# Optimization experiments

Measured on AMD Instinct MI355X. Metric: run time of the kernel, lower is better.

The kernel has to match this reference:

```python
import jax, jax.numpy as jnp
import numpy as np

B, S, D, H = 2, 2048, 1024, 16
DK = D // H

def setup_inputs() -> dict:
    key = jax.random.key(0)
    ks = jax.random.split(key, 8)
    return {
        "query": jax.random.normal(ks[0], (B, S, D), dtype=jnp.float32),
        "key": jax.random.normal(ks[1], (B, S, D), dtype=jnp.float32),
        "value": jax.random.normal(ks[2], (B, S, D), dtype=jnp.float32),
        "mask": jax.random.randint(ks[3], (B, S, S), 0, 2, dtype=jnp.int32),
        "w_q": jax.random.normal(ks[4], (D, D), dtype=jnp.float32) * (D ** -0.5),
        "w_k": jax.random.normal(ks[5], (D, D), dtype=jnp.float32) * (D ** -0.5),
        "w_v": jax.random.normal(ks[6], (D, D), dtype=jnp.float32) * (D ** -0.5),
        "w_o": jax.random.normal(ks[7], (D, D), dtype=jnp.float32) * (D ** -0.5),
    }

def reference(query, key, value, mask, w_q, w_k, w_v, w_o):
    b, s, d = query.shape
    # Linear projections (torch nn.Linear: x @ W.T); here w_* are [out, in]
    Q = jnp.einsum('bsd,ed->bse', query, w_q).reshape(b, s, H, DK).transpose(0, 2, 1, 3)
    K = jnp.einsum('bsd,ed->bse', key, w_k).reshape(b, s, H, DK).transpose(0, 2, 1, 3)
    V = jnp.einsum('bsd,ed->bse', value, w_v).reshape(b, s, H, DK).transpose(0, 2, 1, 3)
    scale = jnp.float32(DK ** 0.5)
    scores = jnp.einsum('bhqd,bhkd->bhqk', Q, K) / scale  # [B,H,S,S]
    scores = jnp.where(mask[:, None, :, :] == 0, jnp.float32(-1e9), scores)
    attn = jax.nn.softmax(scores, axis=-1)  # dropout p=0 -> identity
    out = jnp.einsum('bhqk,bhkd->bhqd', attn, V)  # [B,H,S,DK]
    out = out.transpose(0, 2, 1, 3).reshape(b, s, d)
    return jnp.einsum('bsd,ed->bse', out, w_o)
```

## Files before the change

### kernel.cpp

```cpp
#include <hip/hip_runtime.h>
#include <stdint.h>

#define B_ 2
#define S_ 2048
#define D_ 1024
#define H_ 16
#define DK_ 64

typedef __attribute__((ext_vector_type(8))) short short8;
typedef __attribute__((ext_vector_type(4))) float f32x4;

__device__ __forceinline__ short f2bf(float f) {
    uint32_t u = __float_as_uint(f);
    return (short)((u + 0x7FFFu + ((u >> 16) & 1u)) >> 16);
}

__device__ __forceinline__ float fexp2(float x) {
    float r;
    asm("v_exp_f32 %0, %1" : "=v"(r) : "v"(x));
    return r;
}

__device__ __forceinline__ uint32_t cvt_pk_bf16(float lo, float hi) {
    uint32_t r;
    asm("v_cvt_pk_bf16_f32 %0, %1, %2" : "=v"(r) : "v"(lo), "v"(hi));
    return r;
}

#define GLOAD16(gptr, lptr)                                                      \
    __builtin_amdgcn_global_load_lds(                                            \
        (const __attribute__((address_space(1))) void*)(gptr),                   \
        (__attribute__((address_space(3))) void*)(lptr), 16, 0, 0)

__global__ __launch_bounds__(256) void prep(const float* __restrict__ q,
                                            const float* __restrict__ k,
                                            const float* __restrict__ v,
                                            const float* __restrict__ wq,
                                            const float* __restrict__ wk,
                                            const float* __restrict__ wv,
                                            const float* __restrict__ wo,
                                            const int* __restrict__ mask,
                                            short* __restrict__ qb, short* __restrict__ kb,
                                            short* __restrict__ vb,
                                            short* __restrict__ wqb, short* __restrict__ wkb,
                                            short* __restrict__ wvb, short* __restrict__ wob,
                                            uint32_t* __restrict__ packed,
                                            float* __restrict__ lut) {
    int bid = blockIdx.x;
    int tid = threadIdx.x;
    if (bid < 8192) {
        const float* in;
        short* out;
        int i;
        if (bid < 6144) {
            int sel = bid >> 11;
            i = (bid & 2047) * 256 + tid;
            in = (sel == 0) ? q : (sel == 1) ? k : v;
            out = (sel == 0) ? qb : (sel == 1) ? kb : vb;
        } else {
            int idx = bid - 6144;
            int sel = idx >> 9;
            i = (idx & 511) * 256 + tid;
            in = (sel == 0) ? wq : (sel == 1) ? wk : (sel == 2) ? wv : wo;
            out = (sel == 0) ? wqb : (sel == 1) ? wkb : (sel == 2) ? wvb : wob;
            if (idx == 0 && tid < 64) {
                int e = tid >> 2, r = tid & 3;
                lut[tid] = ((e >> r) & 1) ? 0.0f : -8.0e9f;
            }
        }
        const float4* p = ((const float4*)in) + (size_t)i * 2;
        float4 x = p[0], y = p[1];
        short8 o;
        o[0] = f2bf(x.x); o[1] = f2bf(x.y); o[2] = f2bf(x.z); o[3] = f2bf(x.w);
        o[4] = f2bf(y.x); o[5] = f2bf(y.y); o[6] = f2bf(y.z); o[7] = f2bf(y.w);
        *(((short8*)out) + i) = o;
    } else {
        size_t t = (size_t)(bid - 8192) * 256 + tid;
        int4 m = ((const int4*)mask)[t];
        uint32_t nib = (m.x != 0 ? 1u : 0u) | (m.y != 0 ? 2u : 0u) |
                       (m.z != 0 ? 4u : 0u) | (m.w != 0 ? 8u : 0u);
        int lane = tid & 63;
        uint32_t vv = nib << ((lane & 7) * 4);
        vv |= __shfl_xor(vv, 1);
        vv |= __shfl_xor(vv, 2);
        vv |= __shfl_xor(vv, 4);
        if ((lane & 7) == 0) packed[t >> 3] = vv;
    }
}

#define GEMM_BODY(A, W, C, F32OUT, Mv, Nv, Kv)                                              \
    __shared__ short As[128 * 32];                                                          \
    __shared__ short Bs[128 * 32];                                                          \
    const int tid = threadIdx.x;                                                            \
    const int lane = tid & 63;                                                              \
    const int w = tid >> 6;                                                                 \
    const int wm = w >> 1, wn = w & 1;                                                      \
    const int l_ = blockIdx.x + (blockIdx.y << 3);                                          \
    const int xcd_ = l_ & 7, ii_ = l_ >> 3;                                                 \
    const int mBase = ((xcd_ << 2) + (ii_ >> 3)) * 128;                                     \
    const int nBase = (ii_ & 7) * 128;                                                      \
    f32x4 acc[4][4];                                                                        \
    _Pragma("unroll") for (int i = 0; i < 4; i++)                                           \
        _Pragma("unroll") for (int j = 0; j < 4; j++) acc[i][j] = (f32x4)0.f;               \
    const int srow = lane >> 2;                                                             \
    const int sslot = lane & 3;                                                             \
    for (int k0 = 0; k0 < Kv; k0 += 32) {                                                   \
        _Pragma("unroll") for (int i = 0; i < 2; ++i) {                                     \
            int seg = w * 2 + i;                                                            \
            int row = seg * 16 + srow;                                                      \
            const short* ga = A + (size_t)(mBase + row) * Kv + k0 + sslot * 8;              \
            GLOAD16(ga, (char*)As + seg * 1024);                                            \
            const short* gb = W + (size_t)(nBase + row) * Kv + k0 + sslot * 8;              \
            GLOAD16(gb, (char*)Bs + seg * 1024);                                            \
        }                                                                                   \
        asm volatile("s_waitcnt vmcnt(0)" ::: "memory");                                    \
        __syncthreads();                                                                    \
        short8 af[4], bfv[4];                                                               \
        _Pragma("unroll") for (int mi = 0; mi < 4; mi++)                                    \
            af[mi] = *(const short8*)&As[(wm * 64 + mi * 16 + (lane & 15)) * 32 + (lane >> 4) * 8]; \
        _Pragma("unroll") for (int ni = 0; ni < 4; ni++)                                    \
            bfv[ni] = *(const short8*)&Bs[(wn * 64 + ni * 16 + (lane & 15)) * 32 + (lane >> 4) * 8]; \
        _Pragma("unroll") for (int mi = 0; mi < 4; mi++)                                    \
            _Pragma("unroll") for (int ni = 0; ni < 4; ni++)                                \
                acc[mi][ni] = __builtin_amdgcn_mfma_f32_16x16x32_bf16(af[mi], bfv[ni], acc[mi][ni], 0, 0, 0); \
        __syncthreads();                                                                    \
    }                                                                                       \
    _Pragma("unroll") for (int mi = 0; mi < 4; mi++)                                        \
        _Pragma("unroll") for (int ni = 0; ni < 4; ni++)                                    \
            _Pragma("unroll") for (int r = 0; r < 4; r++) {                                 \
                int row = mBase + wm * 64 + mi * 16 + (lane >> 4) * 4 + r;                  \
                int col = nBase + wn * 64 + ni * 16 + (lane & 15);                          \
                float v = acc[mi][ni][r];                                                   \
                if (F32OUT) ((float*)C)[(size_t)row * Nv + col] = v;                        \
                else        ((short*)C)[(size_t)row * Nv + col] = f2bf(v);                  \
            }

__global__ __launch_bounds__(256) void gemm3_nt(const short* __restrict__ A0, const short* __restrict__ W0, short* __restrict__ C0,
                                                const short* __restrict__ A1, const short* __restrict__ W1, short* __restrict__ C1,
                                                const short* __restrict__ A2, const short* __restrict__ W2, short* __restrict__ C2) {
    const int z = blockIdx.z;
    const short* A = (z == 0) ? A0 : (z == 1) ? A1 : A2;
    const short* W = (z == 0) ? W0 : (z == 1) ? W1 : W2;
    short* C = (z == 0) ? C0 : (z == 1) ? C1 : C2;
    GEMM_BODY(A, W, C, 0, (B_ * S_), D_, D_)
}

__global__ __launch_bounds__(256) void gemm_out(const short* __restrict__ A,
                                                const short* __restrict__ W,
                                                float* __restrict__ C) {
    GEMM_BODY(A, W, C, 1, (B_ * S_), D_, D_)
}

__global__ __launch_bounds__(256) void transpose_v(const short* __restrict__ Vp,
                                                   short* __restrict__ Vt) {
    __shared__ short t[64 * 72];
    int bid = blockIdx.x;
    int bh = bid >> 5;
    int st = bid & 31;
    int b = bh >> 4, h = bh & 15;
    int sBase = st * 64;
    int tid = threadIdx.x;
#pragma unroll
    for (int i = 0; i < 2; i++) {
        int ci = i * 256 + tid;
        int sr = ci >> 3, sl = ci & 7;
        short8 v = *(const short8*)&Vp[(size_t)(b * S_ + sBase + sr) * D_ + h * 64 + sl * 8];
#pragma unroll
        for (int j = 0; j < 8; j++) t[(sl * 8 + j) * 72 + sr] = v[j];
    }
    __syncthreads();
#pragma unroll
    for (int i = 0; i < 2; i++) {
        int ci = i * 256 + tid;
        int dk = ci >> 3, sl = ci & 7;
        short8 o = *(const short8*)&t[dk * 72 + sl * 8];
        *(short8*)&Vt[(size_t)((b * H_ + h) * 64 + dk) * S_ + sBase + sl * 8] = o;
    }
}

__global__ __launch_bounds__(512) void attn_kernel(const short* __restrict__ Qp,
                                                   const short* __restrict__ Kp,
                                                   const short* __restrict__ Vt,
                                                   const uint32_t* __restrict__ mp,
                                                   const float* __restrict__ lutg,
                                                   short* __restrict__ Op) {
    __shared__ short Ks[2][2][64 * 64];
    __shared__ short Vs[2][2][64 * 64];
    const int l_ = blockIdx.x + (blockIdx.y << 4);
    const int bh = ((l_ & 7) << 2) + (l_ >> 7);
    const int qt = (l_ >> 3) & 15;
    const int b = bh >> 4, h = bh & 15;
    const int qBase = qt * 128;
    const int tid = threadIdx.x, lane = tid & 63, w = tid >> 6;
    const int lg = lane >> 4;
    const int li = lane & 15;
    const float c1 = 0.18033688011112042f;

    const int q = qBase + w * 16 + li;

    short8 qf[2];
#pragma unroll
    for (int ks = 0; ks < 2; ks++)
        qf[ks] = *(const short8*)&Qp[(size_t)(b * S_ + q) * D_ + h * 64 + lg * 8 + ks * 32];

    const int r0 = tid >> 3, sl = tid & 7;
    const int gs = sl ^ (r0 & 7);
    const short* kgb = Kp + ((size_t)(b * S_) + r0) * D_ + h * 64 + gs * 8;
    const short* vgb = Vt + ((size_t)bh * 64 + r0) * S_ + gs * 8;
    const uint32_t* mrow = mp + ((size_t)(b * S_) + q) * 64;
    char* ldsK = (char*)&Ks[0][0][0];
    char* ldsV = (char*)&Vs[0][0][0];
    const int woff = w * 1024;

#pragma unroll
    for (int st = 0; st < 2; st++) {
        GLOAD16(kgb + (size_t)(st * 64) * D_, ldsK + st * 8192 + woff);
        GLOAD16(vgb + st * 64, ldsV + st * 8192 + woff);
    }
    uint4 mw4 = *(const uint4*)mrow;
    asm volatile("s_waitcnt vmcnt(0)" ::: "memory");
    __syncthreads();

    float m_r = -1e30f, l_r = 0.f;
    f32x4 acc[4];
#pragma unroll
    for (int g = 0; g < 4; g++) acc[g] = (f32x4)0.f;

    int cur = 0;

    for (int kt = 0; kt < S_ / 128; ++kt) {
        uint32_t mwarr[4] = {mw4.x, mw4.y, mw4.z, mw4.w};
        f32x4 msk[8];
#pragma unroll
        for (int nt = 0; nt < 8; nt++) {
            uint32_t wd = mwarr[nt >> 1];
            uint32_t nib = (wd >> (((nt & 1) << 4) + (lg << 2))) & 0xFu;
            msk[nt] = *(const f32x4*)&lutg[nib * 4];
        }

        uint4 mwn;
        if (kt < S_ / 128 - 1) {
            const int boff = (cur ^ 1) * 16384 + woff;
#pragma unroll
            for (int st = 0; st < 2; st++) {
                const size_t kr = (size_t)((kt + 1) * 128 + st * 64);
                GLOAD16(kgb + kr * D_, ldsK + boff + st * 8192);
                GLOAD16(vgb + kr, ldsV + boff + st * 8192);
            }
            mwn = *(const uint4*)&mrow[(kt + 1) * 4];
        }

        f32x4 sc[8];
        __builtin_amdgcn_s_setprio(1);
#pragma unroll
        for (int st = 0; st < 2; st++)
#pragma unroll
            for (int ntl = 0; ntl < 4; ntl++) {
                f32x4 c = msk[st * 4 + ntl];
#pragma unroll
                for (int ks = 0; ks < 2; ks++) {
                    short8 kf = *(const short8*)&Ks[cur][st][(ntl * 16 + li) * 64 + (((lg + ks * 4) ^ (li & 7)) << 3)];
                    c = __builtin_amdgcn_mfma_f32_16x16x32_bf16(kf, qf[ks], c, 0, 0, 0);
                }
                sc[st * 4 + ntl] = c;
            }
        __builtin_amdgcn_s_setprio(0);

        float t0 = fmaxf(fmaxf(sc[0][0], sc[0][1]), fmaxf(sc[0][2], sc[0][3]));
        float t1 = fmaxf(fmaxf(sc[1][0], sc[1][1]), fmaxf(sc[1][2], sc[1][3]));
        float t2 = fmaxf(fmaxf(sc[2][0], sc[2][1]), fmaxf(sc[2][2], sc[2][3]));
        float t3 = fmaxf(fmaxf(sc[3][0], sc[3][1]), fmaxf(sc[3][2], sc[3][3]));
        float t4 = fmaxf(fmaxf(sc[4][0], sc[4][1]), fmaxf(sc[4][2], sc[4][3]));
        float t5 = fmaxf(fmaxf(sc[5][0], sc[5][1]), fmaxf(sc[5][2], sc[5][3]));
        float t6 = fmaxf(fmaxf(sc[6][0], sc[6][1]), fmaxf(sc[6][2], sc[6][3]));
        float t7 = fmaxf(fmaxf(sc[7][0], sc[7][1]), fmaxf(sc[7][2], sc[7][3]));
        float tm = fmaxf(fmaxf(fmaxf(t0, t1), fmaxf(t2, t3)),
                         fmaxf(fmaxf(t4, t5), fmaxf(t6, t7)));
        tm = fmaxf(tm, __shfl_xor(tm, 16));
        tm = fmaxf(tm, __shfl_xor(tm, 32));

        if (__any((tm - m_r) * c1 > 10.0f)) {
            float mn = fmaxf(m_r, tm);
            float alpha = fexp2((m_r - mn) * c1);
            m_r = mn;
            l_r *= alpha;
#pragma unroll
            for (int g = 0; g < 4; g++) acc[g] *= alpha;
        }
        float mc = m_r * c1;

        uint32_t u[8][2];
        float ls = 0.f;
#pragma unroll
        for (int nt = 0; nt < 8; nt++) {
            float e0 = fexp2(__builtin_fmaf(sc[nt][0], c1, -mc));
            float e1 = fexp2(__builtin_fmaf(sc[nt][1], c1, -mc));
            float e2 = fexp2(__builtin_fmaf(sc[nt][2], c1, -mc));
            float e3 = fexp2(__builtin_fmaf(sc[nt][3], c1, -mc));
            ls += (e0 + e1) + (e2 + e3);
            u[nt][0] = cvt_pk_bf16(e0, e1);
            u[nt][1] = cvt_pk_bf16(e2, e3);
        }
        ls += __shfl_xor(ls, 16);
        ls += __shfl_xor(ls, 32);
        l_r += ls;

        __builtin_amdgcn_s_setprio(1);
#pragma unroll
        for (int ks = 0; ks < 4; ks++) {
            const uint32_t s00 = u[2 * ks][0], s01 = u[2 * ks][1];
            const uint32_t s10 = u[2 * ks + 1][0], s11 = u[2 * ks + 1][1];
            uint32_t e0 = (lg & 1) ? s00 : s10;
            uint32_t e1 = (lg & 1) ? s01 : s11;
            uint32_t x0 = (uint32_t)__shfl_xor((int)e0, 16);
            uint32_t x1 = (uint32_t)__shfl_xor((int)e1, 16);
            union { uint32_t w4[4]; short8 s8; } pu;
            pu.w4[0] = (lg & 1) ? x0 : s00;
            pu.w4[1] = (lg & 1) ? x1 : s01;
            pu.w4[2] = (lg & 1) ? s10 : x0;
            pu.w4[3] = (lg & 1) ? s11 : x1;
            const int f = ks * 4 + ((lg & 1) << 1) + (lg >> 1);
            const int stv = f >> 3, fl = f & 7;
#pragma unroll
            for (int g = 0; g < 4; g++) {
                short8 vf = *(const short8*)&Vs[cur][stv][(g * 16 + li) * 64 + ((fl ^ (li & 7)) << 3)];
                acc[g] = __builtin_amdgcn_mfma_f32_16x16x32_bf16(vf, pu.s8, acc[g], 0, 0, 0);
            }
        }
        __builtin_amdgcn_s_setprio(0);

        asm volatile("s_waitcnt vmcnt(0)" ::: "memory");
        __syncthreads();
        cur ^= 1;
        if (kt < S_ / 128 - 1) mw4 = mwn;
    }

    float inv = 1.f / l_r;
    short* orow = &Op[(size_t)(b * S_ + q) * D_ + h * 64];
#pragma unroll
    for (int g = 0; g < 4; g++) {
        uint2 o;
        o.x = cvt_pk_bf16(acc[g][0] * inv, acc[g][1] * inv);
        o.y = cvt_pk_bf16(acc[g][2] * inv, acc[g][3] * inv);
        *(uint2*)&orow[g * 16 + lg * 4] = o;
    }
}

extern "C" void kernel_launch(void* const* d_in, const int* in_sizes, int n_in,
                              void* d_out, int out_size, void* d_ws, size_t ws_size,
                              hipStream_t stream) {
    const float* q  = (const float*)d_in[0];
    const float* k  = (const float*)d_in[1];
    const float* v  = (const float*)d_in[2];
    const int*   mk = (const int*)d_in[3];
    const float* wq = (const float*)d_in[4];
    const float* wk = (const float*)d_in[5];
    const float* wv = (const float*)d_in[6];
    const float* wo = (const float*)d_in[7];

    const size_t SZ = (size_t)B_ * S_ * D_;
    const size_t DD = (size_t)D_ * D_;
    const size_t NEED = (6 * SZ + 4 * DD) * 2 + (size_t)B_ * S_ * 64 * 4 + 256;
    if (ws_size < NEED) return;

    short* ws  = (short*)d_ws;
    short* qb  = ws;
    short* kb  = qb + SZ;
    short* vb  = kb + SZ;
    short* wqb = vb + SZ;
    short* wkb = wqb + DD;
    short* wvb = wkb + DD;
    short* wob = wvb + DD;
    short* Qp  = wob + DD;
    short* Kp  = Qp + SZ;
    short* Vp  = Kp + SZ;
    uint32_t* mp = (uint32_t*)(Vp + SZ);
    float* lutg = (float*)(mp + (size_t)B_ * S_ * 64);
    short* Vtr = qb;
    short* Opx = kb;

    dim3 blk(256);
    prep<<<dim3(16384), blk, 0, stream>>>(q, k, v, wq, wk, wv, wo, mk,
                                          qb, kb, vb, wqb, wkb, wvb, wob, mp, lutg);

    gemm3_nt<<<dim3(8, 32, 3), blk, 0, stream>>>(qb, wqb, Qp, kb, wkb, Kp, vb, wvb, Vp);

    transpose_v<<<dim3(B_ * H_ * (S_ / 64)), blk, 0, stream>>>(Vp, Vtr);

    attn_kernel<<<dim3(16, 32), dim3(512), 0, stream>>>(Qp, Kp, Vtr, mp, lutg, Opx);

    gemm_out<<<dim3(8, 32), blk, 0, stream>>>(Opx, wob, (float*)d_out);
}
```

Baseline: 170.2 us.

## Process two query row-groups per wave in attention, halving block threads

Each wave in the attention kernel now handles 32 query rows (two 16-row groups) instead of 16, and the block shrinks from 512 to 256 threads while keeping a 128-query tile. Each K and V fragment read from LDS now feeds two MFMAs, which halves LDS read traffic per FLOP. Each thread issues twice the global-to-LDS loads to fill the same tiles. The cost is roughly double the accumulator and score registers per thread, which may cut occupancy or cause spills, and there are fewer waves per block to hide latency.

```diff
diff --git a/kernel.cpp b/kernel.cpp
--- a/kernel.cpp
+++ b/kernel.cpp
@@ -178,7 +178,7 @@
     }
 }
 
-__global__ __launch_bounds__(512) void attn_kernel(const short* __restrict__ Qp,
+__global__ __launch_bounds__(256) void attn_kernel(const short* __restrict__ Qp,
                                                    const short* __restrict__ Kp,
                                                    const short* __restrict__ Vt,
                                                    const uint32_t* __restrict__ mp,
@@ -196,18 +196,22 @@
     const int li = lane & 15;
     const float c1 = 0.18033688011112042f;
 
-    const int q = qBase + w * 16 + li;
-
-    short8 qf[2];
-#pragma unroll
-    for (int ks = 0; ks < 2; ks++)
-        qf[ks] = *(const short8*)&Qp[(size_t)(b * S_ + q) * D_ + h * 64 + lg * 8 + ks * 32];
+    const int qA = qBase + w * 32 + li;
+    const int qB = qA + 16;
+
+    short8 qfA[2], qfB[2];
+#pragma unroll
+    for (int ks = 0; ks < 2; ks++) {
+        qfA[ks] = *(const short8*)&Qp[(size_t)(b * S_ + qA) * D_ + h * 64 + lg * 8 + ks * 32];
+        qfB[ks] = *(const short8*)&Qp[(size_t)(b * S_ + qB) * D_ + h * 64 + lg * 8 + ks * 32];
+    }
 
     const int r0 = tid >> 3, sl = tid & 7;
     const int gs = sl ^ (r0 & 7);
     const short* kgb = Kp + ((size_t)(b * S_) + r0) * D_ + h * 64 + gs * 8;
     const short* vgb = Vt + ((size_t)bh * 64 + r0) * S_ + gs * 8;
-    const uint32_t* mrow = mp + ((size_t)(b * S_) + q) * 64;
+    const uint32_t* mrowA = mp + ((size_t)(b * S_) + qA) * 64;
+    const uint32_t* mrowB = mp + ((size_t)(b * S_) + qB) * 64;
     char* ldsK = (char*)&Ks[0][0][0];
     char* ldsV = (char*)&Vs[0][0][0];
     const int woff = w * 1024;
@@ -215,116 +219,162 @@
 #pragma unroll
     for (int st = 0; st < 2; st++) {
         GLOAD16(kgb + (size_t)(st * 64) * D_, ldsK + st * 8192 + woff);
+        GLOAD16(kgb + (size_t)(st * 64 + 32) * D_, ldsK + st * 8192 + 4096 + woff);
         GLOAD16(vgb + st * 64, ldsV + st * 8192 + woff);
-    }
-    uint4 mw4 = *(const uint4*)mrow;
+        GLOAD16(vgb + st * 64 + (size_t)32 * S_, ldsV + st * 8192 + 4096 + woff);
+    }
+    uint4 mw4a = *(const uint4*)mrowA;
+    uint4 mw4b = *(const uint4*)mrowB;
     asm volatile("s_waitcnt vmcnt(0)" ::: "memory");
     __syncthreads();
 
-    float m_r = -1e30f, l_r = 0.f;
-    f32x4 acc[4];
-#pragma unroll
-    for (int g = 0; g < 4; g++) acc[g] = (f32x4)0.f;
+    float m_rA = -1e30f, l_rA = 0.f, m_rB = -1e30f, l_rB = 0.f;
+    f32x4 accA[4], accB[4];
+#pragma unroll
+    for (int g = 0; g < 4; g++) { accA[g] = (f32x4)0.f; accB[g] = (f32x4)0.f; }
 
     int cur = 0;
 
     for (int kt = 0; kt < S_ / 128; ++kt) {
-        uint32_t mwarr[4] = {mw4.x, mw4.y, mw4.z, mw4.w};
-        f32x4 msk[8];
+        uint32_t mwaA[4] = {mw4a.x, mw4a.y, mw4a.z, mw4a.w};
+        uint32_t mwaB[4] = {mw4b.x, mw4b.y, mw4b.z, mw4b.w};
+        f32x4 mskA[8], mskB[8];
 #pragma unroll
         for (int nt = 0; nt < 8; nt++) {
-            uint32_t wd = mwarr[nt >> 1];
-            uint32_t nib = (wd >> (((nt & 1) << 4) + (lg << 2))) & 0xFu;
-            msk[nt] = *(const f32x4*)&lutg[nib * 4];
-        }
-
-        uint4 mwn;
+            uint32_t sh = ((nt & 1) << 4) + (lg << 2);
+            mskA[nt] = *(const f32x4*)&lutg[((mwaA[nt >> 1] >> sh) & 0xFu) * 4];
+            mskB[nt] = *(const f32x4*)&lutg[((mwaB[nt >> 1] >> sh) & 0xFu) * 4];
+        }
+
+        uint4 mwnA, mwnB;
         if (kt < S_ / 128 - 1) {
             const int boff = (cur ^ 1) * 16384 + woff;
 #pragma unroll
             for (int st = 0; st < 2; st++) {
                 const size_t kr = (size_t)((kt + 1) * 128 + st * 64);
                 GLOAD16(kgb + kr * D_, ldsK + boff + st * 8192);
+                GLOAD16(kgb + (kr + 32) * D_, ldsK + boff + st * 8192 + 4096);
                 GLOAD16(vgb + kr, ldsV + boff + st * 8192);
+                GLOAD16(vgb + kr + (size_t)32 * S_, ldsV + boff + st * 8192 + 4096);
             }
-            mwn = *(const uint4*)&mrow[(kt + 1) * 4];
-        }
-
-        f32x4 sc[8];
+            mwnA = *(const uint4*)&mrowA[(kt + 1) * 4];
+            mwnB = *(const uint4*)&mrowB[(kt + 1) * 4];
+        }
+
+        f32x4 scA[8], scB[8];
         __builtin_amdgcn_s_setprio(1);
 #pragma unroll
         for (int st = 0; st < 2; st++)
 #pragma unroll
             for (int ntl = 0; ntl < 4; ntl++) {
-                f32x4 c = msk[st * 4 + ntl];
+                f32x4 cA = mskA[st * 4 + ntl];
+                f32x4 cB = mskB[st * 4 + ntl];
 #pragma unroll
                 for (int ks = 0; ks < 2; ks++) {
                     short8 kf = *(const short8*)&Ks[cur][st][(ntl * 16 + li) * 64 + (((lg + ks * 4) ^ (li & 7)) << 3)];
-                    c = __builtin_amdgcn_mfma_f32_16x16x32_bf16(kf, qf[ks], c, 0, 0, 0);
+                    cA = __builtin_amdgcn_mfma_f32_16x16x32_bf16(kf, qfA[ks], cA, 0, 0, 0);
+                    cB = __builtin_amdgcn_mfma_f32_16x16x32_bf16(kf, qfB[ks], cB, 0, 0, 0);
                 }
-                sc[st * 4 + ntl] = c;
+                scA[st * 4 + ntl] = cA;
+                scB[st * 4 + ntl] = cB;
             }
         __builtin_amdgcn_s_setprio(0);
 
-        float t0 = fmaxf(fmaxf(sc[0][0], sc[0][1]), fmaxf(sc[0][2], sc[0][3]));
-        float t1 = fmaxf(fmaxf(sc[1][0], sc[1][1]), fmaxf(sc[1][2], sc[1][3]));
-        float t2 = fmaxf(fmaxf(sc[2][0], sc[2][1]), fmaxf(sc[2][2], sc[2][3]));
-        float t3 = fmaxf(fmaxf(sc[3][0], sc[3][1]), fmaxf(sc[3][2], sc[3][3]));
-        float t4 = fmaxf(fmaxf(sc[4][0], sc[4][1]), fmaxf(sc[4][2], sc[4][3]));
-        float t5 = fmaxf(fmaxf(sc[5][0], sc[5][1]), fmaxf(sc[5][2], sc[5][3]));
-        float t6 = fmaxf(fmaxf(sc[6][0], sc[6][1]), fmaxf(sc[6][2], sc[6][3]));
-        float t7 = fmaxf(fmaxf(sc[7][0], sc[7][1]), fmaxf(sc[7][2], sc[7][3]));
-        float tm = fmaxf(fmaxf(fmaxf(t0, t1), fmaxf(t2, t3)),
-                         fmaxf(fmaxf(t4, t5), fmaxf(t6, t7)));
-        tm = fmaxf(tm, __shfl_xor(tm, 16));
-        tm = fmaxf(tm, __shfl_xor(tm, 32));
-
-        if (__any((tm - m_r) * c1 > 10.0f)) {
-            float mn = fmaxf(m_r, tm);
-            float alpha = fexp2((m_r - mn) * c1);
-            m_r = mn;
-            l_r *= alpha;
-#pragma unroll
-            for (int g = 0; g < 4; g++) acc[g] *= alpha;
-        }
-        float mc = m_r * c1;
-
-        uint32_t u[8][2];
-        float ls = 0.f;
+        float a0 = fmaxf(fmaxf(scA[0][0], scA[0][1]), fmaxf(scA[0][2], scA[0][3]));
+        float a1 = fmaxf(fmaxf(scA[1][0], scA[1][1]), fmaxf(scA[1][2], scA[1][3]));
+        float a2 = fmaxf(fmaxf(scA[2][0], scA[2][1]), fmaxf(scA[2][2], scA[2][3]));
+        float a3 = fmaxf(fmaxf(scA[3][0], scA[3][1]), fmaxf(scA[3][2], scA[3][3]));
+        float a4 = fmaxf(fmaxf(scA[4][0], scA[4][1]), fmaxf(scA[4][2], scA[4][3]));
+        float a5 = fmaxf(fmaxf(scA[5][0], scA[5][1]), fmaxf(scA[5][2], scA[5][3]));
+        float a6 = fmaxf(fmaxf(scA[6][0], scA[6][1]), fmaxf(scA[6][2], scA[6][3]));
+        float a7 = fmaxf(fmaxf(scA[7][0], scA[7][1]), fmaxf(scA[7][2], scA[7][3]));
+        float tmA = fmaxf(fmaxf(fmaxf(a0, a1), fmaxf(a2, a3)),
+                          fmaxf(fmaxf(a4, a5), fmaxf(a6, a7)));
+        tmA = fmaxf(tmA, __shfl_xor(tmA, 16));
+        tmA = fmaxf(tmA, __shfl_xor(tmA, 32));
+        float b0 = fmaxf(fmaxf(scB[0][0], scB[0][1]), fmaxf(scB[0][2], scB[0][3]));
+        float b1 = fmaxf(fmaxf(scB[1][0], scB[1][1]), fmaxf(scB[1][2], scB[1][3]));
+        float b2 = fmaxf(fmaxf(scB[2][0], scB[2][1]), fmaxf(scB[2][2], scB[2][3]));
+        float b3 = fmaxf(fmaxf(scB[3][0], scB[3][1]), fmaxf(scB[3][2], scB[3][3]));
+        float b4 = fmaxf(fmaxf(scB[4][0], scB[4][1]), fmaxf(scB[4][2], scB[4][3]));
+        float b5 = fmaxf(fmaxf(scB[5][0], scB[5][1]), fmaxf(scB[5][2], scB[5][3]));
+        float b6 = fmaxf(fmaxf(scB[6][0], scB[6][1]), fmaxf(scB[6][2], scB[6][3]));
+        float b7 = fmaxf(fmaxf(scB[7][0], scB[7][1]), fmaxf(scB[7][2], scB[7][3]));
+        float tmB = fmaxf(fmaxf(fmaxf(b0, b1), fmaxf(b2, b3)),
+                          fmaxf(fmaxf(b4, b5), fmaxf(b6, b7)));
+        tmB = fmaxf(tmB, __shfl_xor(tmB, 16));
+        tmB = fmaxf(tmB, __shfl_xor(tmB, 32));
+
+        if (__any(((tmA - m_rA) * c1 > 10.0f) || ((tmB - m_rB) * c1 > 10.0f))) {
+            float mnA = fmaxf(m_rA, tmA);
+            float alA = fexp2((m_rA - mnA) * c1);
+            m_rA = mnA; l_rA *= alA;
+            float mnB = fmaxf(m_rB, tmB);
+            float alB = fexp2((m_rB - mnB) * c1);
+            m_rB = mnB; l_rB *= alB;
+#pragma unroll
+            for (int g = 0; g < 4; g++) { accA[g] *= alA; accB[g] *= alB; }
+        }
+        float mcA = m_rA * c1, mcB = m_rB * c1;
+
+        uint32_t uA[8][2], uB[8][2];
+        float lsA = 0.f, lsB = 0.f;
 #pragma unroll
         for (int nt = 0; nt < 8; nt++) {
-            float e0 = fexp2(__builtin_fmaf(sc[nt][0], c1, -mc));
-            float e1 = fexp2(__builtin_fmaf(sc[nt][1], c1, -mc));
-            float e2 = fexp2(__builtin_fmaf(sc[nt][2], c1, -mc));
-            float e3 = fexp2(__builtin_fmaf(sc[nt][3], c1, -mc));
-            ls += (e0 + e1) + (e2 + e3);
-            u[nt][0] = cvt_pk_bf16(e0, e1);
-            u[nt][1] = cvt_pk_bf16(e2, e3);
-        }
-        ls += __shfl_xor(ls, 16);
-        ls += __shfl_xor(ls, 32);
-        l_r += ls;
+            float e0 = fexp2(__builtin_fmaf(scA[nt][0], c1, -mcA));
+            float e1 = fexp2(__builtin_fmaf(scA[nt][1], c1, -mcA));
+            float e2 = fexp2(__builtin_fmaf(scA[nt][2], c1, -mcA));
+            float e3 = fexp2(__builtin_fmaf(scA[nt][3], c1, -mcA));
+            lsA += (e0 + e1) + (e2 + e3);
+            uA[nt][0] = cvt_pk_bf16(e0, e1);
+            uA[nt][1] = cvt_pk_bf16(e2, e3);
+            float f0 = fexp2(__builtin_fmaf(scB[nt][0], c1, -mcB));
+            float f1 = fexp2(__builtin_fmaf(scB[nt][1], c1, -mcB));
+            float f2 = fexp2(__builtin_fmaf(scB[nt][2], c1, -mcB));
+            float f3 = fexp2(__builtin_fmaf(scB[nt][3], c1, -mcB));
+            lsB += (f0 + f1) + (f2 + f3);
+            uB[nt][0] = cvt_pk_bf16(f0, f1);
+            uB[nt][1] = cvt_pk_bf16(f2, f3);
+        }
+        lsA += __shfl_xor(lsA, 16);
+        lsA += __shfl_xor(lsA, 32);
+        l_rA += lsA;
+        lsB += __shfl_xor(lsB, 16);
+        lsB += __shfl_xor(lsB, 32);
+        l_rB += lsB;
 
         __builtin_amdgcn_s_setprio(1);
 #pragma unroll
         for (int ks = 0; ks < 4; ks++) {
-            const uint32_t s00 = u[2 * ks][0], s01 = u[2 * ks][1];
-            const uint32_t s10 = u[2 * ks + 1][0], s11 = u[2 * ks + 1][1];
-            uint32_t e0 = (lg & 1) ? s00 : s10;
-            uint32_t e1 = (lg & 1) ? s01 : s11;
-            uint32_t x0 = (uint32_t)__shfl_xor((int)e0, 16);
-            uint32_t x1 = (uint32_t)__shfl_xor((int)e1, 16);
-            union { uint32_t w4[4]; short8 s8; } pu;
-            pu.w4[0] = (lg & 1) ? x0 : s00;
-            pu.w4[1] = (lg & 1) ? x1 : s01;
-            pu.w4[2] = (lg & 1) ? s10 : x0;
-            pu.w4[3] = (lg & 1) ? s11 : x1;
+            const uint32_t sA00 = uA[2 * ks][0], sA01 = uA[2 * ks][1];
+            const uint32_t sA10 = uA[2 * ks + 1][0], sA11 = uA[2 * ks + 1][1];
+            uint32_t eA0 = (lg & 1) ? sA00 : sA10;
+            uint32_t eA1 = (lg & 1) ? sA01 : sA11;
+            uint32_t xA0 = (uint32_t)__shfl_xor((int)eA0, 16);
+            uint32_t xA1 = (uint32_t)__shfl_xor((int)eA1, 16);
+            union { uint32_t w4[4]; short8 s8; } puA;
+            puA.w4[0] = (lg & 1) ? xA0 : sA00;
+            puA.w4[1] = (lg & 1) ? xA1 : sA01;
+            puA.w4[2] = (lg & 1) ? sA10 : xA0;
+            puA.w4[3] = (lg & 1) ? sA11 : xA1;
+            const uint32_t sB00 = uB[2 * ks][0], sB01 = uB[2 * ks][1];
+            const uint32_t sB10 = uB[2 * ks + 1][0], sB11 = uB[2 * ks + 1][1];
+            uint32_t eB0 = (lg & 1) ? sB00 : sB10;
+            uint32_t eB1 = (lg & 1) ? sB01 : sB11;
+            uint32_t xB0 = (uint32_t)__shfl_xor((int)eB0, 16);
+            uint32_t xB1 = (uint32_t)__shfl_xor((int)eB1, 16);
+            union { uint32_t w4[4]; short8 s8; } puB;
+            puB.w4[0] = (lg & 1) ? xB0 : sB00;
+            puB.w4[1] = (lg & 1) ? xB1 : sB01;
+            puB.w4[2] = (lg & 1) ? sB10 : xB0;
+            puB.w4[3] = (lg & 1) ? sB11 : xB1;
             const int f = ks * 4 + ((lg & 1) << 1) + (lg >> 1);
             const int stv = f >> 3, fl = f & 7;
 #pragma unroll
             for (int g = 0; g < 4; g++) {
                 short8 vf = *(const short8*)&Vs[cur][stv][(g * 16 + li) * 64 + ((fl ^ (li & 7)) << 3)];
-                acc[g] = __builtin_amdgcn_mfma_f32_16x16x32_bf16(vf, pu.s8, acc[g], 0, 0, 0);
+                accA[g] = __builtin_amdgcn_mfma_f32_16x16x32_bf16(vf, puA.s8, accA[g], 0, 0, 0);
+                accB[g] = __builtin_amdgcn_mfma_f32_16x16x32_bf16(vf, puB.s8, accB[g], 0, 0, 0);
             }
         }
         __builtin_amdgcn_s_setprio(0);
@@ -332,17 +382,21 @@
         asm volatile("s_waitcnt vmcnt(0)" ::: "memory");
         __syncthreads();
         cur ^= 1;
-        if (kt < S_ / 128 - 1) mw4 = mwn;
-    }
-
-    float inv = 1.f / l_r;
-    short* orow = &Op[(size_t)(b * S_ + q) * D_ + h * 64];
+        if (kt < S_ / 128 - 1) { mw4a = mwnA; mw4b = mwnB; }
+    }
+
+    float invA = 1.f / l_rA, invB = 1.f / l_rB;
+    short* orowA = &Op[(size_t)(b * S_ + qA) * D_ + h * 64];
+    short* orowB = &Op[(size_t)(b * S_ + qB) * D_ + h * 64];
 #pragma unroll
     for (int g = 0; g < 4; g++) {
-        uint2 o;
-        o.x = cvt_pk_bf16(acc[g][0] * inv, acc[g][1] * inv);
-        o.y = cvt_pk_bf16(acc[g][2] * inv, acc[g][3] * inv);
-        *(uint2*)&orow[g * 16 + lg * 4] = o;
+        uint2 oa, ob;
+        oa.x = cvt_pk_bf16(accA[g][0] * invA, accA[g][1] * invA);
+        oa.y = cvt_pk_bf16(accA[g][2] * invA, accA[g][3] * invA);
+        *(uint2*)&orowA[g * 16 + lg * 4] = oa;
+        ob.x = cvt_pk_bf16(accB[g][0] * invB, accB[g][1] * invB);
+        ob.y = cvt_pk_bf16(accB[g][2] * invB, accB[g][3] * invB);
+        *(uint2*)&orowB[g * 16 + lg * 4] = ob;
     }
 }
 
@@ -387,7 +441,7 @@
 
     transpose_v<<<dim3(B_ * H_ * (S_ / 64)), blk, 0, stream>>>(Vp, Vtr);
 
-    attn_kernel<<<dim3(16, 32), dim3(512), 0, stream>>>(Qp, Kp, Vtr, mp, lutg, Opx);
+    attn_kernel<<<dim3(16, 32), dim3(256), 0, stream>>>(Qp, Kp, Vtr, mp, lutg, Opx);
 
     gemm_out<<<dim3(8, 32), blk, 0, stream>>>(Opx, wob, (float*)d_out);
 }
```

Result: faster. 157.0 us (-7.8%).
